# Performance work log

Measured on AMD Instinct MI355X. Metric: run time of the kernel, lower is better.

Reference implementation:

```python
import jax, jax.numpy as jnp
import numpy as np
from jax import lax

EPS = 1e-06
PAD = 1


def setup_inputs() -> dict:
    key = jax.random.key(0)
    k1, k2, k3, k4, k5 = jax.random.split(key, 5)
    B, C, H, W = 16, 512, 64, 64  # in_channels == out_channels (required by the module's broadcast)
    w_dim, ksz = 512, 3
    x = jax.random.normal(k1, (B, C, H, W), dtype=jnp.float32)
    w = jax.random.normal(k2, (B, w_dim), dtype=jnp.float32)
    conv_weight = jax.random.normal(k3, (C, C, ksz, ksz), dtype=jnp.float32)
    # nn.Linear(w_dim, out_channels): weight (out, in), bias (out), default uniform init
    bound = 1.0 / np.sqrt(w_dim)
    linear_w = jax.random.uniform(k4, (C, w_dim), minval=-bound, maxval=bound, dtype=jnp.float32)
    linear_b = jax.random.uniform(k5, (C,), minval=-bound, maxval=bound, dtype=jnp.float32)
    return {"x": x, "w": w, "conv_weight": conv_weight, "linear_w": linear_w, "linear_b": linear_b}


def reference(x, w, conv_weight, linear_w, linear_b):
    B, Cin, H, W = x.shape
    # style_scale = Linear(w): (B, out_channels)
    style = jnp.einsum('bd,od->bo', w, linear_w) + linear_b
    # modulate: (1, out, in, k, k) * (B, 1, out, 1, 1)  [requires in == out, as in the source]
    w_prime = conv_weight[None] * style[:, None, :, None, None]
    # demodulate over (in, kh, kw)
    denom = jnp.sqrt(jnp.sum(w_prime ** 2, axis=(2, 3, 4), keepdims=True) + EPS)
    w_pp = w_prime / denom  # (B, out, in, k, k)
    Cout = w_pp.shape[2]
    ksz = w_pp.shape[3]
    # grouped conv trick: fold batch into channels, groups = B
    eff_x = x.reshape(1, B * Cin, H, W)
    eff_f = w_pp.reshape(B * Cout, Cin, ksz, ksz)
    out = lax.conv_general_dilated(
        eff_x, eff_f,
        window_strides=(1, 1),
        padding=[(PAD, PAD), (PAD, PAD)],
        dimension_numbers=('NCHW', 'OIHW', 'NCHW'),
        feature_group_count=B,
    )
    return out.reshape(B, Cout, H, W)
```

## Files before the change

### kernel.cpp

```cpp
#include <hip/hip_runtime.h>

typedef unsigned short ushort_t;
typedef unsigned int uint_t;
typedef __bf16 bf16x8 __attribute__((ext_vector_type(8)));
typedef float float4v __attribute__((ext_vector_type(4)));
typedef uint_t uint4v __attribute__((ext_vector_type(4)));
typedef uint_t uint2v __attribute__((ext_vector_type(2)));

#define EPS 1e-6f

#define WS_STYLE   0
#define WS_INVD    32768
#define WS_WSQ     65536
#define WS_AW      1114112
#define WS_XP      6291456

__device__ __forceinline__ ushort_t f2bf(float v) {
    union { float f; uint_t u; } c; c.f = v;
    uint_t u = c.u;
    u += 0x7fffu + ((u >> 16) & 1u);
    return (ushort_t)(u >> 16);
}

__device__ __forceinline__ void gload_lds16(const void* g, void* l) {
    __builtin_amdgcn_global_load_lds(
        (const __attribute__((address_space(1))) uint_t*)g,
        (__attribute__((address_space(3))) uint_t*)l, 16, 0, 0);
}

__global__ void prep_fused1(const float* __restrict__ w, const float* __restrict__ lw,
                            const float* __restrict__ lb, const float* __restrict__ cw,
                            float* __restrict__ style, ushort_t* __restrict__ Aw,
                            float* __restrict__ wsq) {
    int blk = blockIdx.x;
    if (blk < 2048) {
        int gw = blk * 4 + (threadIdx.x >> 6);
        int lane = threadIdx.x & 63;
        int b = gw >> 9, o = gw & 511;
        float s = 0.f;
#pragma unroll
        for (int j = 0; j < 8; ++j) {
            int d = j * 64 + lane;
            s += w[b * 512 + d] * lw[o * 512 + d];
        }
#pragma unroll
        for (int off = 32; off; off >>= 1) s += __shfl_down(s, off);
        if (lane == 0) style[gw] = s + lb[o];
    } else {
        int id = (blk - 2048) * 256 + threadIdx.x;
        int o = id >> 9, i = id & 511;
        const float* p = cw + (size_t)id * 9;
        size_t base = (size_t)o * 4608 + (size_t)(i >> 6) * 576 + (i & 63);
        float s = 0.f;
#pragma unroll
        for (int t = 0; t < 9; ++t) {
            float v = p[t];
            s += v * v;
            Aw[base + t * 64] = f2bf(v);
        }
        wsq[id] = s;
    }
}

__global__ void prep_fused2(const float* __restrict__ wsq, const float* __restrict__ style,
                            float* __restrict__ invd, const float* __restrict__ x,
                            ushort_t* __restrict__ Xp) {
    __shared__ ushort_t tile[64][66];
    int blk = blockIdx.x;
    if (blk < 2048) {
        int gw = blk * 4 + (threadIdx.x >> 6);
        int lane = threadIdx.x & 63;
        int b = gw >> 9, o = gw & 511;
        float s = 0.f;
#pragma unroll
        for (int j = 0; j < 8; ++j) {
            int d = j * 64 + lane;
            float st = style[b * 512 + d];
            s += wsq[o * 512 + d] * st * st;
        }
#pragma unroll
        for (int off = 32; off; off >>= 1) s += __shfl_down(s, off);
        if (lane == 0) invd[gw] = rsqrtf(s + EPS);
    } else if (blk < 3088) {
        int j = (blk - 2048) * 4 + (threadIdx.x >> 6);
        int lane = threadIdx.x & 63;
        int b = j / 260, bp = j - b * 260;
        int py, px;
        if (bp < 66)       { py = 0;        px = bp; }
        else if (bp < 132) { py = 65;       px = bp - 66; }
        else if (bp < 196) { py = bp - 131; px = 0; }
        else               { py = bp - 195; px = 65; }
        size_t pix = ((size_t)b * 66 + py) * 66 + px;
        ((uint4v*)(Xp + pix * 512))[lane] = (uint4v){0, 0, 0, 0};
    } else {
        int mb = blk - 3088;
        int y = mb & 63;
        int chunk = mb >> 6;
        int i0 = (chunk & 7) * 64;
        int b = chunk >> 3;
        int tid = threadIdx.x;
        int ch = tid >> 2;
        int xq = tid & 3;
        float s = style[b * 512 + i0 + ch];
        const float* xrow = x + (((size_t)b * 512 + i0 + ch) * 64 + y) * 64;
#pragma unroll
        for (int pass = 0; pass < 4; ++pass) {
            int x0 = pass * 16 + xq * 4;
            float4v v = *(const float4v*)(xrow + x0);
            ushort_t u[4];
#pragma unroll
            for (int j = 0; j < 4; ++j) u[j] = f2bf(v[j] * s);
            *(uint2v*)(&tile[ch][x0]) = *(const uint2v*)u;
        }
        __syncthreads();
        size_t rowbase = ((size_t)b * 66 + (y + 1)) * 66 + 1;
#pragma unroll
        for (int pass = 0; pass < 2; ++pass) {
            int idx = pass * 256 + tid;
            int xx = idx >> 3;
            int ch8 = idx & 7;
            ushort_t v[8];
#pragma unroll
            for (int j = 0; j < 8; ++j) v[j] = tile[ch8 * 8 + j][xx];
            *(uint4v*)(Xp + (rowbase + xx) * 512 + i0 + ch8 * 8) = *(uint4v*)v;
        }
    }
}

__global__ __launch_bounds__(512, 2) void conv_gemm(const ushort_t* __restrict__ Aw,
                                                    const ushort_t* __restrict__ Xp,
                                                    const float* __restrict__ invd,
                                                    float* __restrict__ out) {
    __shared__ ushort_t lds[2][32768];

    const int tid  = threadIdx.x;
    const int lane = tid & 63;
    const int wv   = tid >> 6;
    const int wm   = wv >> 2;
    const int wn   = wv & 3;
    const int l15  = lane & 15;
    const int quad = lane >> 4;

    const int bid = blockIdx.x;
    const int xcd = bid & 7;
    const int ci  = bid >> 3;
    const int b   = xcd * 2 + (ci >> 5);
    const int ot  = (ci >> 4) & 1;
    const int pxt = ci & 15;
    const int o0  = ot * 256;
    const int p0  = pxt * 256;

    const int tr  = tid >> 3;
    const int gsw = (((tid & 7) ^ (tr & 7)) << 4);
    const char* aga0 = (const char*)Aw + (size_t)(o0 + tr) * 9216 + gsw;
    const char* bga0 = (const char*)Xp + ((size_t)(b * 66 + pxt * 4) * 66 + tr) * 1024 + gsw;
    const int lds_wv = wv * 1024;

    const int sw0 = ((quad ^ (l15 & 7)) << 4);
    const int sw1 = (((4 + quad) ^ (l15 & 7)) << 4);
    const int aoffs = (wm * 128 + l15) * 128;
    const int boffs = 32768 + (wn * 64 + l15) * 128;

    float4v acc[8][4] = {};
    bf16x8 a0[8], b0[4], a1[8], b1[4];

    auto stage = [&](int kt2) {
        const int parity = kt2 & 1;
        const long aoff = (long)kt2 * 128;
        const int iblk = (kt2 * 7282) >> 16;
        const int t = kt2 - iblk * 9;
        const int dh = t / 3, dw = t - dh * 3;
        const long boff = (long)(dh * 66 + dw) * 1024 + (long)iblk * 128;
        char* la = (char*)&lds[parity][0]     + lds_wv;
        char* lb = (char*)&lds[parity][16384] + lds_wv;
#pragma unroll
        for (int s = 0; s < 4; ++s) {
            gload_lds16(aga0 + (size_t)s * 589824 + aoff, la + s * 8192);
            gload_lds16(bga0 + (size_t)s * 67584  + boff, lb + s * 8192);
        }
    };

    stage(0);
    stage(1);
    asm volatile("s_waitcnt vmcnt(8)" ::: "memory");
    __builtin_amdgcn_s_barrier();
    {
        const char* base = (const char*)&lds[0][0];
#pragma unroll
        for (int ni = 0; ni < 4; ++ni) b0[ni] = *(const bf16x8*)(base + boffs + ni * 2048 + sw0);
#pragma unroll
        for (int mi = 0; mi < 8; ++mi) a0[mi] = *(const bf16x8*)(base + aoffs + mi * 2048 + sw0);
    }

#pragma unroll 1
    for (int kt = 0; kt < 72; ++kt) {
        const char* cbase = (const char*)&lds[kt & 1][0];

#pragma unroll
        for (int ni = 0; ni < 4; ++ni) b1[ni] = *(const bf16x8*)(cbase + boffs + ni * 2048 + sw1);
#pragma unroll
        for (int mi = 0; mi < 8; ++mi) a1[mi] = *(const bf16x8*)(cbase + aoffs + mi * 2048 + sw1);

        __builtin_amdgcn_s_setprio(1);
#pragma unroll
        for (int mi = 0; mi < 8; ++mi)
#pragma unroll
            for (int ni = 0; ni < 4; ++ni)
                acc[mi][ni] = __builtin_amdgcn_mfma_f32_16x16x32_bf16(a0[mi], b0[ni], acc[mi][ni], 0, 0, 0);
        __builtin_amdgcn_s_setprio(0);

        asm volatile("s_waitcnt lgkmcnt(0)" ::: "memory");
        asm volatile("s_waitcnt vmcnt(0)" ::: "memory");
        __builtin_amdgcn_s_barrier();

        if (kt < 71) {
            const char* nbase = (const char*)&lds[(kt + 1) & 1][0];
#pragma unroll
            for (int ni = 0; ni < 4; ++ni) b0[ni] = *(const bf16x8*)(nbase + boffs + ni * 2048 + sw0);
#pragma unroll
            for (int mi = 0; mi < 8; ++mi) a0[mi] = *(const bf16x8*)(nbase + aoffs + mi * 2048 + sw0);
        }
        if (kt < 70) stage(kt + 2);

        __builtin_amdgcn_s_setprio(1);
#pragma unroll
        for (int mi = 0; mi < 8; ++mi)
#pragma unroll
            for (int ni = 0; ni < 4; ++ni)
                acc[mi][ni] = __builtin_amdgcn_mfma_f32_16x16x32_bf16(a1[mi], b1[ni], acc[mi][ni], 0, 0, 0);
        __builtin_amdgcn_s_setprio(0);
    }

    const float* invb = invd + b * 512 + o0 + wm * 128;
    float* outb = out + ((size_t)b * 512 + o0 + wm * 128) * 4096 + p0 + wn * 64;
#pragma unroll
    for (int mi = 0; mi < 8; ++mi) {
#pragma unroll
        for (int r = 0; r < 4; ++r) {
            int m = mi * 16 + quad * 4 + r;
            float d = invb[m];
#pragma unroll
            for (int ni = 0; ni < 4; ++ni) {
                int n = ni * 16 + l15;
                outb[(size_t)m * 4096 + n] = acc[mi][ni][r] * d;
            }
        }
    }
}

extern "C" void kernel_launch(void* const* d_in, const int* in_sizes, int n_in,
                              void* d_out, int out_size, void* d_ws, size_t ws_size,
                              hipStream_t stream) {
    const float* x  = (const float*)d_in[0];
    const float* w  = (const float*)d_in[1];
    const float* cw = (const float*)d_in[2];
    const float* lw = (const float*)d_in[3];
    const float* lb = (const float*)d_in[4];
    float* out = (float*)d_out;

    char* ws = (char*)d_ws;
    float*    style = (float*)(ws + WS_STYLE);
    float*    invd  = (float*)(ws + WS_INVD);
    float*    wsq   = (float*)(ws + WS_WSQ);
    ushort_t* Aw    = (ushort_t*)(ws + WS_AW);
    ushort_t* Xp    = (ushort_t*)(ws + WS_XP);

    prep_fused1<<<3072, 256, 0, stream>>>(w, lw, lb, cw, style, Aw, wsq);
    prep_fused2<<<11280, 256, 0, stream>>>(wsq, style, invd, x, Xp);
    conv_gemm<<<512, 512, 0, stream>>>(Aw, Xp, invd, out);
}
```

Measured before the change: 471.4 us.

## Split A fragments into halves and interleave LDS reads with MFMA quarters

Replaces the two full sets of A/B register fragments with half-size A buffers, issuing LDS reads for the next quarter while the current quarter's MFMAs run, with sched_barriers fencing the order. This is meant to cut VGPR pressure and hide LDS latency behind compute at finer granularity. The prologue now waits for all global loads (vmcnt(0)) instead of leaving one stage in flight. The next stage's global prefetch is issued before the next-tile register reads. The fixed scheduling barriers may stop the compiler from reordering profitably, and the stricter prologue wait adds a small startup stall.

Measured after the change: 484.4 us. 1.03x slower.

```diff
diff --git a/kernel.cpp b/kernel.cpp
--- a/kernel.cpp
+++ b/kernel.cpp
@@ -162,7 +162,7 @@
     const int boffs = 32768 + (wn * 64 + l15) * 128;
 
     float4v acc[8][4] = {};
-    bf16x8 a0[8], b0[4], a1[8], b1[4];
+    bf16x8 aC[4], aN[4], bC[4], bN[4];
 
     auto stage = [&](int kt2) {
         const int parity = kt2 & 1;
@@ -180,55 +180,65 @@
         }
     };
 
+    auto RD_A = [&](bf16x8 (&av)[4], const char* base, int h, int sw) {
+#pragma unroll
+        for (int j = 0; j < 4; ++j)
+            av[j] = *(const bf16x8*)(base + aoffs + (h * 4 + j) * 2048 + sw);
+    };
+    auto RD_B = [&](bf16x8 (&bv)[4], const char* base, int sw) {
+#pragma unroll
+        for (int j = 0; j < 4; ++j)
+            bv[j] = *(const bf16x8*)(base + boffs + j * 2048 + sw);
+    };
+    auto MFMA16 = [&](bf16x8 (&av)[4], bf16x8 (&bv)[4], int h) {
+        __builtin_amdgcn_s_setprio(1);
+#pragma unroll
+        for (int mi = 0; mi < 4; ++mi)
+#pragma unroll
+            for (int ni = 0; ni < 4; ++ni)
+                acc[h * 4 + mi][ni] =
+                    __builtin_amdgcn_mfma_f32_16x16x32_bf16(av[mi], bv[ni], acc[h * 4 + mi][ni], 0, 0, 0);
+        __builtin_amdgcn_s_setprio(0);
+    };
+
     stage(0);
     stage(1);
-    asm volatile("s_waitcnt vmcnt(8)" ::: "memory");
+    asm volatile("s_waitcnt vmcnt(0)" ::: "memory");
     __builtin_amdgcn_s_barrier();
     {
-        const char* base = (const char*)&lds[0][0];
-#pragma unroll
-        for (int ni = 0; ni < 4; ++ni) b0[ni] = *(const bf16x8*)(base + boffs + ni * 2048 + sw0);
-#pragma unroll
-        for (int mi = 0; mi < 8; ++mi) a0[mi] = *(const bf16x8*)(base + aoffs + mi * 2048 + sw0);
+        const char* b0p = (const char*)&lds[0][0];
+        RD_A(aC, b0p, 0, sw0);
+        RD_B(bC, b0p, sw0);
     }
 
 #pragma unroll 1
     for (int kt = 0; kt < 72; ++kt) {
-        const char* cbase = (const char*)&lds[kt & 1][0];
-
-#pragma unroll
-        for (int ni = 0; ni < 4; ++ni) b1[ni] = *(const bf16x8*)(cbase + boffs + ni * 2048 + sw1);
-#pragma unroll
-        for (int mi = 0; mi < 8; ++mi) a1[mi] = *(const bf16x8*)(cbase + aoffs + mi * 2048 + sw1);
-
-        __builtin_amdgcn_s_setprio(1);
-#pragma unroll
-        for (int mi = 0; mi < 8; ++mi)
-#pragma unroll
-            for (int ni = 0; ni < 4; ++ni)
-                acc[mi][ni] = __builtin_amdgcn_mfma_f32_16x16x32_bf16(a0[mi], b0[ni], acc[mi][ni], 0, 0, 0);
-        __builtin_amdgcn_s_setprio(0);
+        const char* cb = (const char*)&lds[kt & 1][0];
+
+        RD_A(aN, cb, 1, sw0);
+        __builtin_amdgcn_sched_barrier(0);
+        MFMA16(aC, bC, 0);
+
+        RD_A(aC, cb, 0, sw1);
+        RD_B(bN, cb, sw1);
+        __builtin_amdgcn_sched_barrier(0);
+        MFMA16(aN, bC, 1);
+
+        RD_A(aN, cb, 1, sw1);
+        __builtin_amdgcn_sched_barrier(0);
+        MFMA16(aC, bN, 0);
 
         asm volatile("s_waitcnt lgkmcnt(0)" ::: "memory");
         asm volatile("s_waitcnt vmcnt(0)" ::: "memory");
         __builtin_amdgcn_s_barrier();
-
+        if (kt < 70) stage(kt + 2);
         if (kt < 71) {
-            const char* nbase = (const char*)&lds[(kt + 1) & 1][0];
-#pragma unroll
-            for (int ni = 0; ni < 4; ++ni) b0[ni] = *(const bf16x8*)(nbase + boffs + ni * 2048 + sw0);
-#pragma unroll
-            for (int mi = 0; mi < 8; ++mi) a0[mi] = *(const bf16x8*)(nbase + aoffs + mi * 2048 + sw0);
-        }
-        if (kt < 70) stage(kt + 2);
-
-        __builtin_amdgcn_s_setprio(1);
-#pragma unroll
-        for (int mi = 0; mi < 8; ++mi)
-#pragma unroll
-            for (int ni = 0; ni < 4; ++ni)
-                acc[mi][ni] = __builtin_amdgcn_mfma_f32_16x16x32_bf16(a1[mi], b1[ni], acc[mi][ni], 0, 0, 0);
-        __builtin_amdgcn_s_setprio(0);
+            const char* nb = (const char*)&lds[(kt + 1) & 1][0];
+            RD_A(aC, nb, 0, sw0);
+            RD_B(bC, nb, sw0);
+        }
+        __builtin_amdgcn_sched_barrier(0);
+        MFMA16(aN, bN, 1);
     }
 
     const float* invb = invd + b * 512 + o0 + wm * 128;
```

## Shrink conv GEMM tile to 256x128 with K=64 steps and simpler double buffering

Applied to the files above, without the earlier changes.

The implicit-GEMM conv kernel moves from 512-thread blocks with 256x256 output tiles and K=128 stages to 256-thread blocks with 256x128 tiles and K=64 stages, launching twice as many blocks. LDS per block drops from 128KB to 48KB, the swizzle is changed for 64-wide rows, and the register double-buffered fragment prefetch is replaced by a plain load-then-compute loop with one stage of global prefetch. The aim is more resident blocks and smaller per-block footprint, but it reduces operand reuse per tile, doubles barrier count, and loses the overlap of LDS reads with MFMA.

After: 541.0 us. 1.15x slower.

```diff
diff --git a/kernel.cpp b/kernel.cpp
--- a/kernel.cpp
+++ b/kernel.cpp
@@ -127,108 +127,93 @@
     }
 }
 
-__global__ __launch_bounds__(512, 2) void conv_gemm(const ushort_t* __restrict__ Aw,
+__global__ __launch_bounds__(256, 2) void conv_gemm(const ushort_t* __restrict__ Aw,
                                                     const ushort_t* __restrict__ Xp,
                                                     const float* __restrict__ invd,
                                                     float* __restrict__ out) {
-    __shared__ ushort_t lds[2][32768];
+    __shared__ ushort_t As[2][8192];
+    __shared__ ushort_t Bs[2][4096];
 
     const int tid  = threadIdx.x;
     const int lane = tid & 63;
     const int wv   = tid >> 6;
-    const int wm   = wv >> 2;
-    const int wn   = wv & 3;
+    const int wm   = wv >> 1;
+    const int wn   = wv & 1;
     const int l15  = lane & 15;
     const int quad = lane >> 4;
 
     const int bid = blockIdx.x;
     const int xcd = bid & 7;
     const int ci  = bid >> 3;
-    const int b   = xcd * 2 + (ci >> 5);
-    const int ot  = (ci >> 4) & 1;
-    const int pxt = ci & 15;
+    const int b   = xcd * 2 + (ci >> 6);
+    const int ot  = (ci >> 5) & 1;
+    const int pt  = ci & 31;
     const int o0  = ot * 256;
-    const int p0  = pxt * 256;
-
-    const int tr  = tid >> 3;
-    const int gsw = (((tid & 7) ^ (tr & 7)) << 4);
-    const char* aga0 = (const char*)Aw + (size_t)(o0 + tr) * 9216 + gsw;
-    const char* bga0 = (const char*)Xp + ((size_t)(b * 66 + pxt * 4) * 66 + tr) * 1024 + gsw;
+    const int p0  = pt * 128;
+
+    const int tr4 = tid >> 2;
+    const int gsw = (((tid & 3) ^ ((tr4 ^ (tr4 >> 2)) & 3)) << 4);
+    const char* aga0 = (const char*)Aw + (size_t)(o0 + tr4) * 9216 + gsw;
+    const char* bga0 = (const char*)Xp + ((size_t)(b * 66 + pt * 2) * 66 + tr4) * 1024 + gsw;
     const int lds_wv = wv * 1024;
 
-    const int sw0 = ((quad ^ (l15 & 7)) << 4);
-    const int sw1 = (((4 + quad) ^ (l15 & 7)) << 4);
-    const int aoffs = (wm * 128 + l15) * 128;
-    const int boffs = 32768 + (wn * 64 + l15) * 128;
+    const int sw    = ((quad ^ ((l15 ^ (l15 >> 2)) & 3)) << 4);
+    const int aoffs = (wm * 128 + l15) * 64;
+    const int boffs = (wn * 64 + l15) * 64;
 
     float4v acc[8][4] = {};
-    bf16x8 a0[8], b0[4], a1[8], b1[4];
 
     auto stage = [&](int kt2) {
         const int parity = kt2 & 1;
-        const long aoff = (long)kt2 * 128;
-        const int iblk = (kt2 * 7282) >> 16;
-        const int t = kt2 - iblk * 9;
-        const int dh = t / 3, dw = t - dh * 3;
-        const long boff = (long)(dh * 66 + dw) * 1024 + (long)iblk * 128;
-        char* la = (char*)&lds[parity][0]     + lds_wv;
-        char* lb = (char*)&lds[parity][16384] + lds_wv;
-#pragma unroll
-        for (int s = 0; s < 4; ++s) {
-            gload_lds16(aga0 + (size_t)s * 589824 + aoff, la + s * 8192);
-            gload_lds16(bga0 + (size_t)s * 67584  + boff, lb + s * 8192);
-        }
+        const int iblk = (kt2 * 3641) >> 16;
+        const int rem  = kt2 - iblk * 18;
+        const int t    = rem >> 1;
+        const int h    = rem & 1;
+        const int dh   = (t * 11) >> 5;
+        const int dw   = t - dh * 3;
+        const long aoff = (long)kt2 * 64;
+        const long boff = (long)(dh * 66 + dw) * 1024 + iblk * 128 + h * 64;
+        char* la = (char*)&As[parity][0] + lds_wv;
+        char* lb = (char*)&Bs[parity][0] + lds_wv;
+#pragma unroll
+        for (int s = 0; s < 4; ++s)
+            gload_lds16(aga0 + (size_t)s * 589824 + aoff, la + s * 4096);
+#pragma unroll
+        for (int s = 0; s < 2; ++s)
+            gload_lds16(bga0 + (size_t)s * 67584 + boff, lb + s * 4096);
     };
 
     stage(0);
-    stage(1);
-    asm volatile("s_waitcnt vmcnt(8)" ::: "memory");
-    __builtin_amdgcn_s_barrier();
-    {
-        const char* base = (const char*)&lds[0][0];
-#pragma unroll
-        for (int ni = 0; ni < 4; ++ni) b0[ni] = *(const bf16x8*)(base + boffs + ni * 2048 + sw0);
-#pragma unroll
-        for (int mi = 0; mi < 8; ++mi) a0[mi] = *(const bf16x8*)(base + aoffs + mi * 2048 + sw0);
-    }
 
 #pragma unroll 1
-    for (int kt = 0; kt < 72; ++kt) {
-        const char* cbase = (const char*)&lds[kt & 1][0];
-
-#pragma unroll
-        for (int ni = 0; ni < 4; ++ni) b1[ni] = *(const bf16x8*)(cbase + boffs + ni * 2048 + sw1);
-#pragma unroll
-        for (int mi = 0; mi < 8; ++mi) a1[mi] = *(const bf16x8*)(cbase + aoffs + mi * 2048 + sw1);
+    for (int kt = 0; kt < 144; ++kt) {
+        if (kt < 143) {
+            stage(kt + 1);
+            asm volatile("s_waitcnt vmcnt(6)" ::: "memory");
+        } else {
+            asm volatile("s_waitcnt vmcnt(0)" ::: "memory");
+        }
+        __builtin_amdgcn_s_barrier();
+
+        const char* ab = (const char*)&As[kt & 1][0];
+        const char* bb = (const char*)&Bs[kt & 1][0];
+        bf16x8 av[8], bv[4];
+#pragma unroll
+        for (int mi = 0; mi < 8; ++mi)
+            av[mi] = *(const bf16x8*)(ab + aoffs + mi * 1024 + sw);
+#pragma unroll
+        for (int ni = 0; ni < 4; ++ni)
+            bv[ni] = *(const bf16x8*)(bb + boffs + ni * 1024 + sw);
 
         __builtin_amdgcn_s_setprio(1);
 #pragma unroll
         for (int mi = 0; mi < 8; ++mi)
 #pragma unroll
             for (int ni = 0; ni < 4; ++ni)
-                acc[mi][ni] = __builtin_amdgcn_mfma_f32_16x16x32_bf16(a0[mi], b0[ni], acc[mi][ni], 0, 0, 0);
+                acc[mi][ni] = __builtin_amdgcn_mfma_f32_16x16x32_bf16(av[mi], bv[ni], acc[mi][ni], 0, 0, 0);
         __builtin_amdgcn_s_setprio(0);
 
-        asm volatile("s_waitcnt lgkmcnt(0)" ::: "memory");
-        asm volatile("s_waitcnt vmcnt(0)" ::: "memory");
         __builtin_amdgcn_s_barrier();
-
-        if (kt < 71) {
-            const char* nbase = (const char*)&lds[(kt + 1) & 1][0];
-#pragma unroll
-            for (int ni = 0; ni < 4; ++ni) b0[ni] = *(const bf16x8*)(nbase + boffs + ni * 2048 + sw0);
-#pragma unroll
-            for (int mi = 0; mi < 8; ++mi) a0[mi] = *(const bf16x8*)(nbase + aoffs + mi * 2048 + sw0);
-        }
-        if (kt < 70) stage(kt + 2);
-
-        __builtin_amdgcn_s_setprio(1);
-#pragma unroll
-        for (int mi = 0; mi < 8; ++mi)
-#pragma unroll
-            for (int ni = 0; ni < 4; ++ni)
-                acc[mi][ni] = __builtin_amdgcn_mfma_f32_16x16x32_bf16(a1[mi], b1[ni], acc[mi][ni], 0, 0, 0);
-        __builtin_amdgcn_s_setprio(0);
     }
 
     const float* invb = invd + b * 512 + o0 + wm * 128;
@@ -267,5 +252,5 @@
 
     prep_fused1<<<3072, 256, 0, stream>>>(w, lw, lb, cw, style, Aw, wsq);
     prep_fused2<<<11280, 256, 0, stream>>>(wsq, style, invd, x, Xp);
-    conv_gemm<<<512, 512, 0, stream>>>(Aw, Xp, invd, out);
-}
+    conv_gemm<<<1024, 256, 0, stream>>>(Aw, Xp, invd, out);
+}
```
